# Performance work log

Hardware: AMD Instinct MI355X
Metric: run time of the kernel (lower is better)

Reference implementation:

```python
import jax, jax.numpy as jnp
import numpy as np

B, K_LEN, D = 16, 2048, 512
TEMP_EPS = 1e-06   # episilon added to temperature in the torch code
LN_EPS = 1e-05     # nn.LayerNorm default eps
NEG_INF = -10000000000.0


def setup_inputs() -> dict:
    key = jax.random.key(0)
    kq, kk, kv, km, kwq, kwk, kwv = jax.random.split(key, 7)
    std = np.sqrt(2.0 / D).astype(np.float32)
    return {
        "Q": jax.random.normal(kq, (B, D), dtype=jnp.float32),
        "K": jax.random.normal(kk, (B, K_LEN, D), dtype=jnp.float32),
        "V": jax.random.normal(kv, (B, K_LEN, D), dtype=jnp.float32),
        "mask": jax.random.randint(km, (B, K_LEN), 0, 2).astype(bool),
        "W_q": jax.random.normal(kwq, (D, D), dtype=jnp.float32) * std,
        "W_k": jax.random.normal(kwk, (D, D), dtype=jnp.float32) * std,
        "W_v": jax.random.normal(kwv, (D, D), dtype=jnp.float32) * std,
        "ln_gamma": jnp.ones((D,), dtype=jnp.float32),
        "ln_beta": jnp.zeros((D,), dtype=jnp.float32),
    }


def _layer_norm(x, gamma, beta):
    mu = jnp.mean(x, axis=-1, keepdims=True)
    var = jnp.mean(jnp.square(x - mu), axis=-1, keepdims=True)
    return (x - mu) * jax.lax.rsqrt(var + LN_EPS) * gamma + beta


def reference(Q, K, V, mask, W_q, W_k, W_v, ln_gamma, ln_beta):
    # Q: (B, D) -> unsqueeze to (B, 1, D); K, V: (B, K_LEN, D); mask: (B, K_LEN) bool
    d = Q.shape[-1]
    k_len = K.shape[1]
    temperature = d ** 0.5 + TEMP_EPS

    Q_ = Q[:, None, :] @ W_q            # (B, 1, D)
    K_ = K @ W_k                        # (B, K_LEN, D)
    V_ = V @ W_v                        # (B, K_LEN, D)

    scores = jnp.einsum('bqd,bkd->bqk', Q_, K_) / temperature   # (B, 1, K_LEN)
    # torch: Q_K.repeat(1, k_len, 1) -> every query row is the same score row
    Q_K = jnp.broadcast_to(scores, (Q.shape[0], k_len, k_len))  # (B, K_LEN, K_LEN)

    # mask_ = triu(ones, diag=1) OR pad_mask (pad mask broadcast over keys)
    causal = jnp.triu(jnp.ones((k_len, k_len), dtype=bool), k=1)  # (K_LEN, K_LEN)
    mask_ = causal[None, :, :] | mask[:, :, None]                 # (B, K_LEN, K_LEN)
    Q_K = jnp.where(mask_, NEG_INF, Q_K)

    att = jax.nn.softmax(Q_K, axis=-1)   # dropout is identity in eval mode
    V_att = att @ V_                     # (B, K_LEN, D)

    return _layer_norm(V + V_att, ln_gamma, ln_beta)
```

## Files before the change

### kernel.cpp

```cpp
#include <hip/hip_runtime.h>
#include <stdint.h>

typedef unsigned short u16;
typedef __attribute__((ext_vector_type(8))) short short8v;
typedef __attribute__((ext_vector_type(4))) float f32x4;

#define NBATCH 16
#define KLEN 2048
#define DDIM 512
#define NTILE 64
#define TROWS 32
#define TEMP_INV (1.0f / 22.627418f)

static __device__ __forceinline__ u16 f2bf(float f) {
  union { float f; uint32_t u; } a; a.f = f;
  uint32_t r = a.u + 0x7FFFu + ((a.u >> 16) & 1u);
  return (u16)(r >> 16);
}
static __device__ __forceinline__ float bf2f(u16 h) {
  union { uint32_t u; float f; } a; a.u = ((uint32_t)h) << 16;
  return a.f;
}

__global__ __launch_bounds__(512) void k_qu(const float* __restrict__ Q,
    const float* __restrict__ Wq, const float* __restrict__ Wk,
    float* __restrict__ u) {
  int b = blockIdx.x, t = threadIdx.x;
  __shared__ float qs[DDIM];
  __shared__ float q2[DDIM];
  qs[t] = Q[b * DDIM + t];
  __syncthreads();
  {
    float acc = 0.f;
    for (int e = 0; e < DDIM; ++e) acc = fmaf(qs[e], Wq[e * DDIM + t], acc);
    q2[t] = acc;
  }
  __syncthreads();
  {
    float acc = 0.f;
    const float* row = Wk + t * DDIM;
    for (int d0 = 0; d0 < DDIM; d0 += 4) {
      float4 wv = *reinterpret_cast<const float4*>(row + d0);
      acc = fmaf(wv.x, q2[d0], acc);
      acc = fmaf(wv.y, q2[d0 + 1], acc);
      acc = fmaf(wv.z, q2[d0 + 2], acc);
      acc = fmaf(wv.w, q2[d0 + 3], acc);
    }
    u[b * DDIM + t] = acc;
  }
}

__global__ void k_wswz(const float* __restrict__ Wv, u16* __restrict__ Wf) {
  int blk = blockIdx.x;
  int l = threadIdx.x;
  int kb = blk >> 5, ni = blk & 31;
  int n = ni * 16 + (l & 15);
  int k0 = kb * 32 + (l >> 4) * 8;
  union { short8v v; u16 s[8]; } tmp;
#pragma unroll
  for (int j = 0; j < 8; ++j) tmp.s[j] = f2bf(Wv[(k0 + j) * DDIM + n]);
  *reinterpret_cast<short8v*>(Wf + (blk * 64 + l) * 8) = tmp.v;
}

__global__ __launch_bounds__(256) void k_scores(const float* __restrict__ Kin,
    const float* __restrict__ u, float* __restrict__ s) {
  int wid = threadIdx.x >> 6, lane = threadIdx.x & 63;
  int row = blockIdx.x * 4 + wid;
  int b = row >> 11;
  const float* kr = Kin + row * DDIM + lane * 8;
  const float* ur = u + b * DDIM + lane * 8;
  float4 k0 = *reinterpret_cast<const float4*>(kr);
  float4 k1 = *reinterpret_cast<const float4*>(kr + 4);
  float4 u0 = *reinterpret_cast<const float4*>(ur);
  float4 u1 = *reinterpret_cast<const float4*>(ur + 4);
  float dot = k0.x * u0.x + k0.y * u0.y + k0.z * u0.z + k0.w * u0.w
            + k1.x * u1.x + k1.y * u1.y + k1.z * u1.z + k1.w * u1.w;
#pragma unroll
  for (int off = 32; off; off >>= 1) dot += __shfl_xor(dot, off);
  if (lane == 0) s[row] = dot * TEMP_INV;
}

__global__ __launch_bounds__(256) void k_expw(const float* __restrict__ s,
    float* __restrict__ w) {
  int b = blockIdx.x, t = threadIdx.x;
  __shared__ float red[4];
  float v[8];
  float m = -3e38f;
#pragma unroll
  for (int i = 0; i < 8; ++i) { v[i] = s[b * KLEN + t * 8 + i]; m = fmaxf(m, v[i]); }
#pragma unroll
  for (int off = 32; off; off >>= 1) m = fmaxf(m, __shfl_xor(m, off));
  if ((t & 63) == 0) red[t >> 6] = m;
  __syncthreads();
  float M = fmaxf(fmaxf(red[0], red[1]), fmaxf(red[2], red[3]));
#pragma unroll
  for (int i = 0; i < 8; ++i) w[b * KLEN + t * 8 + i] = __expf(v[i] - M);
}

__global__ __launch_bounds__(256, 2) void k_gemm(const float* __restrict__ V,
    const u16* __restrict__ Wf, u16* __restrict__ Vp) {
  int rt = blockIdx.x;
  int ct = blockIdx.y;
  __shared__ __align__(16) u16 Asm[4096];
  __shared__ __align__(16) u16 Bsm[4096];
  int t = threadIdx.x;
  int wid = t >> 6, lane = t & 63;
  int wm = wid >> 1, wn = wid & 1;

  f32x4 zero4 = {0.f, 0.f, 0.f, 0.f};
  f32x4 acc[4][4];
#pragma unroll
  for (int i = 0; i < 4; ++i)
#pragma unroll
    for (int j = 0; j < 4; ++j) acc[i][j] = zero4;

  int m_ = t >> 2;
  int k0_ = (t & 3) * 8;
  const float* Abase = V + rt * 128 * DDIM;

  for (int kb = 0; kb < 16; ++kb) {
    __syncthreads();
#pragma unroll
    for (int half = 0; half < 2; ++half) {
      int mm = m_ + half * 64;
      const float* src = Abase + mm * DDIM + kb * 32 + k0_;
      float4 f0 = *reinterpret_cast<const float4*>(src);
      float4 f1 = *reinterpret_cast<const float4*>(src + 4);
      union { short8v v; u16 sb[8]; } tmp;
      tmp.sb[0] = f2bf(f0.x); tmp.sb[1] = f2bf(f0.y);
      tmp.sb[2] = f2bf(f0.z); tmp.sb[3] = f2bf(f0.w);
      tmp.sb[4] = f2bf(f1.x); tmp.sb[5] = f2bf(f1.y);
      tmp.sb[6] = f2bf(f1.z); tmp.sb[7] = f2bf(f1.w);
      int idx = (((mm >> 4) << 6) + ((t & 3) << 4) + (mm & 15)) << 3;
      *reinterpret_cast<short8v*>(&Asm[idx]) = tmp.v;
    }
    {
      int i2 = t;
      *reinterpret_cast<short8v*>(&Bsm[i2 * 8]) =
          *reinterpret_cast<const short8v*>(Wf + ((kb * 32 + ct * 8) * 64 + i2) * 8);
      i2 = t + 256;
      *reinterpret_cast<short8v*>(&Bsm[i2 * 8]) =
          *reinterpret_cast<const short8v*>(Wf + ((kb * 32 + ct * 8) * 64 + i2) * 8);
    }
    __syncthreads();
    short8v af[4], bfr[4];
#pragma unroll
    for (int i = 0; i < 4; ++i)
      af[i] = *reinterpret_cast<const short8v*>(&Asm[((wm * 4 + i) * 64 + lane) * 8]);
#pragma unroll
    for (int j = 0; j < 4; ++j)
      bfr[j] = *reinterpret_cast<const short8v*>(&Bsm[((wn * 4 + j) * 64 + lane) * 8]);
#pragma unroll
    for (int i = 0; i < 4; ++i)
#pragma unroll
      for (int j = 0; j < 4; ++j)
        acc[i][j] = __builtin_amdgcn_mfma_f32_16x16x32_bf16(af[i], bfr[j], acc[i][j], 0, 0, 0);
  }
  int r0 = rt * 128 + wm * 64;
  int c0 = ct * 128 + wn * 64;
#pragma unroll
  for (int i = 0; i < 4; ++i)
#pragma unroll
    for (int j = 0; j < 4; ++j)
#pragma unroll
      for (int r = 0; r < 4; ++r) {
        int row = r0 + i * 16 + (lane >> 4) * 4 + r;
        int col = c0 + j * 16 + (lane & 15);
        Vp[row * DDIM + col] = f2bf(acc[i][j][r]);
      }
}

__global__ __launch_bounds__(512) void k_tilesum(const u16* __restrict__ Vp,
    const float* __restrict__ w, float* __restrict__ S, float* __restrict__ U,
    float* __restrict__ z) {
  int bt = blockIdx.x;
  int d = threadIdx.x;
  int krow0 = bt * TROWS;
  const float* wrow = w + krow0;
  const u16* vbase = Vp + krow0 * DDIM + d;
  float Sa = 0.f, Ua = 0.f, za = 0.f;
#pragma unroll 4
  for (int r = 0; r < TROWS; ++r) {
    float wk = wrow[r];
    float v = bf2f(vbase[r * DDIM]);
    Sa = fmaf(wk, v, Sa);
    Ua += v;
    za += wk;
  }
  S[bt * DDIM + d] = Sa;
  U[bt * DDIM + d] = Ua;
  if (d == 0) z[bt] = za;
}

__global__ __launch_bounds__(512) void k_prefix(const float* __restrict__ S,
    const float* __restrict__ U, const float* __restrict__ z,
    float* __restrict__ base_, float* __restrict__ zbase,
    float* __restrict__ meanVp) {
  int b = blockIdx.x, d = threadIdx.x;
  float acc = 0.f, tot = 0.f, zacc = 0.f;
  for (int tt = 0; tt < NTILE; ++tt) {
    int bt = b * NTILE + tt;
    base_[bt * DDIM + d] = acc;
    if (d == 0) zbase[bt] = zacc;
    acc += S[bt * DDIM + d];
    zacc += z[bt];
    tot += U[bt * DDIM + d];
  }
  meanVp[b * DDIM + d] = tot * (1.0f / KLEN);
}

__global__ __launch_bounds__(512, 2) void k_scan(const u16* __restrict__ Vp,
    const float* __restrict__ Vin, const float* __restrict__ w,
    const int* __restrict__ mask, const float* __restrict__ base_,
    const float* __restrict__ zbase, const float* __restrict__ meanVp,
    const float* __restrict__ gamma, const float* __restrict__ beta,
    float* __restrict__ out) {
  int bt = blockIdx.x;
  int b = bt >> 6;
  int d = threadIdx.x;
  __shared__ float xs[TROWS][DDIM];
  float acc = base_[bt * DDIM + d];
  float zacc = zbase[bt];
  float mv = meanVp[b * DDIM + d];
  int krow0 = bt * TROWS;
  for (int r = 0; r < TROWS; ++r) {
    int k = krow0 + r;
    float wk = w[k];
    zacc += wk;
    float v_ = bf2f(Vp[k * DDIM + d]);
    acc = fmaf(wk, v_, acc);
    float vatt = mask[k] ? mv : acc * __builtin_amdgcn_rcpf(zacc);
    xs[r][d] = Vin[k * DDIM + d] + vatt;
  }
  __syncthreads();
  int wid = d >> 6, lane = d & 63;
  float4 g0 = *reinterpret_cast<const float4*>(gamma + lane * 4);
  float4 g1 = *reinterpret_cast<const float4*>(gamma + 256 + lane * 4);
  float4 b0 = *reinterpret_cast<const float4*>(beta + lane * 4);
  float4 b1 = *reinterpret_cast<const float4*>(beta + 256 + lane * 4);
#pragma unroll
  for (int rr = 0; rr < 4; ++rr) {
    int r = wid * 4 + rr;
    float4 x0 = *reinterpret_cast<const float4*>(&xs[r][lane * 4]);
    float4 x1 = *reinterpret_cast<const float4*>(&xs[r][256 + lane * 4]);
    float sum = x0.x + x0.y + x0.z + x0.w + x1.x + x1.y + x1.z + x1.w;
    float sq = x0.x * x0.x + x0.y * x0.y + x0.z * x0.z + x0.w * x0.w
             + x1.x * x1.x + x1.y * x1.y + x1.z * x1.z + x1.w * x1.w;
#pragma unroll
    for (int off = 32; off; off >>= 1) {
      sum += __shfl_xor(sum, off);
      sq += __shfl_xor(sq, off);
    }
    float mu = sum * (1.0f / DDIM);
    float var = sq * (1.0f / DDIM) - mu * mu;
    float rstd = rsqrtf(var + 1e-5f);
    int k = krow0 + r;
    float* orow = out + k * DDIM;
    float4 o0, o1;
    o0.x = (x0.x - mu) * rstd * g0.x + b0.x;
    o0.y = (x0.y - mu) * rstd * g0.y + b0.y;
    o0.z = (x0.z - mu) * rstd * g0.z + b0.z;
    o0.w = (x0.w - mu) * rstd * g0.w + b0.w;
    o1.x = (x1.x - mu) * rstd * g1.x + b1.x;
    o1.y = (x1.y - mu) * rstd * g1.y + b1.y;
    o1.z = (x1.z - mu) * rstd * g1.z + b1.z;
    o1.w = (x1.w - mu) * rstd * g1.w + b1.w;
    *reinterpret_cast<float4*>(orow + lane * 4) = o0;
    *reinterpret_cast<float4*>(orow + 256 + lane * 4) = o1;
  }
}

extern "C" void kernel_launch(void* const* d_in, const int* in_sizes, int n_in,
                              void* d_out, int out_size, void* d_ws, size_t ws_size,
                              hipStream_t stream) {
  const float* Q     = (const float*)d_in[0];
  const float* Kin   = (const float*)d_in[1];
  const float* Vin   = (const float*)d_in[2];
  const int*   mask  = (const int*)d_in[3];
  const float* Wq    = (const float*)d_in[4];
  const float* Wk    = (const float*)d_in[5];
  const float* Wv    = (const float*)d_in[6];
  const float* gamma = (const float*)d_in[7];
  const float* beta  = (const float*)d_in[8];
  float* out = (float*)d_out;

  char* p = (char*)d_ws;
  float* u      = (float*)p; p += NBATCH * DDIM * 4;
  u16*   Wf     = (u16*)p;   p += DDIM * DDIM * 2;
  float* s      = (float*)p; p += NBATCH * KLEN * 4;
  float* w      = (float*)p; p += NBATCH * KLEN * 4;
  float* S      = (float*)p; p += NBATCH * NTILE * DDIM * 4;
  float* U      = (float*)p; p += NBATCH * NTILE * DDIM * 4;
  float* base_  = (float*)p; p += NBATCH * NTILE * DDIM * 4;
  float* z      = (float*)p; p += NBATCH * NTILE * 4;
  float* zbase  = (float*)p; p += NBATCH * NTILE * 4;
  float* meanVp = (float*)p; p += NBATCH * DDIM * 4;
  u16*   Vp     = (u16*)p;   p += (size_t)NBATCH * KLEN * DDIM * 2;

  k_qu<<<NBATCH, 512, 0, stream>>>(Q, Wq, Wk, u);
  k_wswz<<<512, 64, 0, stream>>>(Wv, Wf);
  k_scores<<<(NBATCH * KLEN) / 4, 256, 0, stream>>>(Kin, u, s);
  k_expw<<<NBATCH, 256, 0, stream>>>(s, w);
  k_gemm<<<dim3(256, 4), 256, 0, stream>>>(Vin, Wf, Vp);
  k_tilesum<<<NBATCH * NTILE, 512, 0, stream>>>(Vp, w, S, U, z);
  k_prefix<<<NBATCH, 512, 0, stream>>>(S, U, z, base_, zbase, meanVp);
  k_scan<<<NBATCH * NTILE, 512, 0, stream>>>(Vp, Vin, w, mask, base_, zbase,
                                             meanVp, gamma, beta, out);
}
```

Baseline: 295.7 us.

## Split query projection into parallel kernels and widen prefix-scan grid

The single 16-block kernel that computed Q@W_q and then W_k@q is replaced by two kernels. The first tiles W_q across 64 blocks, reuses each weight load across all 16 batches, and reduces partial sums with atomics into a memset buffer. The second computes each W_k row dot with one wavefront per output and a shuffle reduction. The prefix kernel is also spread from 16 blocks of 512 threads to 128 blocks of 64 threads to use more CUs. This adds a memset and an extra launch, and the atomic accumulation makes the float summation order nondeterministic.

```diff
diff --git a/kernel.cpp b/kernel.cpp
--- a/kernel.cpp
+++ b/kernel.cpp
@@ -22,32 +22,46 @@
   return a.f;
 }
 
-__global__ __launch_bounds__(512) void k_qu(const float* __restrict__ Q,
-    const float* __restrict__ Wq, const float* __restrict__ Wk,
-    float* __restrict__ u) {
-  int b = blockIdx.x, t = threadIdx.x;
-  __shared__ float qs[DDIM];
-  __shared__ float q2[DDIM];
-  qs[t] = Q[b * DDIM + t];
+__global__ __launch_bounds__(64) void k_qu1(const float* __restrict__ Q,
+    const float* __restrict__ Wq, float* __restrict__ q2) {
+  int dc = blockIdx.x & 7, ec = blockIdx.x >> 3;
+  int lane = threadIdx.x;
+  int d = dc * 64 + lane;
+  __shared__ float Qs[NBATCH][64];
+  for (int i = lane; i < NBATCH * 64; i += 64) {
+    int b = i >> 6, e = i & 63;
+    Qs[b][e] = Q[b * DDIM + ec * 64 + e];
+  }
   __syncthreads();
-  {
-    float acc = 0.f;
-    for (int e = 0; e < DDIM; ++e) acc = fmaf(qs[e], Wq[e * DDIM + t], acc);
-    q2[t] = acc;
-  }
-  __syncthreads();
-  {
-    float acc = 0.f;
-    const float* row = Wk + t * DDIM;
-    for (int d0 = 0; d0 < DDIM; d0 += 4) {
-      float4 wv = *reinterpret_cast<const float4*>(row + d0);
-      acc = fmaf(wv.x, q2[d0], acc);
-      acc = fmaf(wv.y, q2[d0 + 1], acc);
-      acc = fmaf(wv.z, q2[d0 + 2], acc);
-      acc = fmaf(wv.w, q2[d0 + 3], acc);
-    }
-    u[b * DDIM + t] = acc;
-  }
+  float acc[NBATCH];
+#pragma unroll
+  for (int b = 0; b < NBATCH; ++b) acc[b] = 0.f;
+#pragma unroll 4
+  for (int e = 0; e < 64; ++e) {
+    float wq = Wq[(ec * 64 + e) * DDIM + d];
+#pragma unroll
+    for (int b = 0; b < NBATCH; ++b) acc[b] = fmaf(Qs[b][e], wq, acc[b]);
+  }
+#pragma unroll
+  for (int b = 0; b < NBATCH; ++b) atomicAdd(&q2[b * DDIM + d], acc[b]);
+}
+
+__global__ __launch_bounds__(256) void k_qu2(const float* __restrict__ q2,
+    const float* __restrict__ Wk, float* __restrict__ u) {
+  int wid = threadIdx.x >> 6, lane = threadIdx.x & 63;
+  int idx = blockIdx.x * 4 + wid;
+  int b = idx >> 9, e = idx & 511;
+  const float* wr = Wk + e * DDIM + lane * 8;
+  const float* qr = q2 + b * DDIM + lane * 8;
+  float4 w0 = *reinterpret_cast<const float4*>(wr);
+  float4 w1 = *reinterpret_cast<const float4*>(wr + 4);
+  float4 p0 = *reinterpret_cast<const float4*>(qr);
+  float4 p1 = *reinterpret_cast<const float4*>(qr + 4);
+  float dot = w0.x * p0.x + w0.y * p0.y + w0.z * p0.z + w0.w * p0.w
+            + w1.x * p1.x + w1.y * p1.y + w1.z * p1.z + w1.w * p1.w;
+#pragma unroll
+  for (int off = 32; off; off >>= 1) dot += __shfl_xor(dot, off);
+  if (lane == 0) u[b * DDIM + e] = dot;
 }
 
 __global__ void k_wswz(const float* __restrict__ Wv, u16* __restrict__ Wf) {
@@ -192,16 +206,18 @@
   if (d == 0) z[bt] = za;
 }
 
-__global__ __launch_bounds__(512) void k_prefix(const float* __restrict__ S,
+__global__ __launch_bounds__(64) void k_prefix(const float* __restrict__ S,
     const float* __restrict__ U, const float* __restrict__ z,
     float* __restrict__ base_, float* __restrict__ zbase,
     float* __restrict__ meanVp) {
-  int b = blockIdx.x, d = threadIdx.x;
+  int b = blockIdx.x >> 3;
+  int dc = blockIdx.x & 7;
+  int d = dc * 64 + threadIdx.x;
   float acc = 0.f, tot = 0.f, zacc = 0.f;
   for (int tt = 0; tt < NTILE; ++tt) {
     int bt = b * NTILE + tt;
     base_[bt * DDIM + d] = acc;
-    if (d == 0) zbase[bt] = zacc;
+    if (dc == 0 && threadIdx.x == 0) zbase[bt] = zacc;
     acc += S[bt * DDIM + d];
     zacc += z[bt];
     tot += U[bt * DDIM + d];
@@ -285,6 +301,7 @@
   float* out = (float*)d_out;
 
   char* p = (char*)d_ws;
+  float* q2     = (float*)p; p += NBATCH * DDIM * 4;
   float* u      = (float*)p; p += NBATCH * DDIM * 4;
   u16*   Wf     = (u16*)p;   p += DDIM * DDIM * 2;
   float* s      = (float*)p; p += NBATCH * KLEN * 4;
@@ -297,13 +314,15 @@
   float* meanVp = (float*)p; p += NBATCH * DDIM * 4;
   u16*   Vp     = (u16*)p;   p += (size_t)NBATCH * KLEN * DDIM * 2;
 
-  k_qu<<<NBATCH, 512, 0, stream>>>(Q, Wq, Wk, u);
+  hipMemsetAsync(q2, 0, NBATCH * DDIM * 4, stream);
+  k_qu1<<<64, 64, 0, stream>>>(Q, Wq, q2);
+  k_qu2<<<(NBATCH * DDIM) / 4, 256, 0, stream>>>(q2, Wk, u);
   k_wswz<<<512, 64, 0, stream>>>(Wv, Wf);
   k_scores<<<(NBATCH * KLEN) / 4, 256, 0, stream>>>(Kin, u, s);
   k_expw<<<NBATCH, 256, 0, stream>>>(s, w);
   k_gemm<<<dim3(256, 4), 256, 0, stream>>>(Vin, Wf, Vp);
   k_tilesum<<<NBATCH * NTILE, 512, 0, stream>>>(Vp, w, S, U, z);
-  k_prefix<<<NBATCH, 512, 0, stream>>>(S, U, z, base_, zbase, meanVp);
+  k_prefix<<<128, 64, 0, stream>>>(S, U, z, base_, zbase, meanVp);
   k_scan<<<NBATCH * NTILE, 512, 0, stream>>>(Vp, Vin, w, mask, base_, zbase,
                                              meanVp, gamma, beta, out);
 }
```

After: 263.8 us. 10.8% less time.
